# Kernel tuning notes

Hardware: AMD Instinct MI355X
Metric: run time of the kernel (lower is better)

## Reference

```python
import jax, jax.numpy as jnp
import numpy as np

N, NODE_IN, EDGE_IN, H, ROUNDS = 768, 64, 32, 128, 2


def setup_inputs() -> dict:
    key = jax.random.key(0)
    ks = jax.random.split(key, 12)
    node_feats = jax.random.normal(ks[0], (N, NODE_IN), dtype=jnp.float32)
    edge_feats = jax.random.normal(ks[1], (N, N, EDGE_IN), dtype=jnp.float32)
    adj_mask = jax.random.randint(ks[2], (N, N), 0, 2).astype(jnp.float32)
    def lin(k, fan_in, fan_out):
        w = jax.random.normal(k, (fan_in, fan_out), dtype=jnp.float32) / jnp.sqrt(fan_in)
        return w
    return {
        "node_feats": node_feats,
        "edge_feats": edge_feats,
        "adj_mask": adj_mask,
        "Wn": lin(ks[3], NODE_IN, H), "bn": jnp.zeros((H,), jnp.float32),
        "We": lin(ks[4], EDGE_IN, H), "be": jnp.zeros((H,), jnp.float32),
        "Wa": lin(ks[5], 2 * H, H), "ba": jnp.zeros((H,), jnp.float32),
        "Wu": lin(ks[6], 2 * H, H), "bu": jnp.zeros((H,), jnp.float32),
    }


def reference(node_feats, edge_feats, adj_mask, Wn, bn, We, be, Wa, ba, Wu, bu):
    relu = jax.nn.relu
    h = relu(node_feats @ Wn + bn)                      # (N, H)
    e = relu(jnp.einsum('ijf,fk->ijk', edge_feats, We) + be)  # (N, N, H)
    deg = jnp.clip(adj_mask.sum(axis=0), 1.0)[:, None]  # (N, 1) receiver degree
    # Precompute edge contribution to agg_lin once (constant across rounds):
    # concat([sender, e]) @ Wa == sender @ Wa[:H] + e @ Wa[H:]
    e_proj = jnp.einsum('ijh,hk->ijk', e, Wa[H:])       # (N, N, H)
    for _ in range(ROUNDS):
        s_proj = h @ Wa[:H]                              # (N, H) sender part
        msgs = relu(s_proj[:, None, :] + e_proj + ba)    # (N, N, H)
        agg = jnp.einsum('ijk,ij->jk', msgs, adj_mask) / deg  # masked sum over senders i
        h = relu(jnp.concatenate([h, agg], axis=-1) @ Wu + bu)
    graph_emb = h.mean(axis=0)
    return (h, graph_emb)
```

## Files before the change

### kernel.cpp

```cpp
#include <hip/hip_runtime.h>
#include <hip/hip_bf16.h>


typedef __bf16 bf16x8 __attribute__((ext_vector_type(8)));
typedef float f32x4 __attribute__((ext_vector_type(4)));

#define NN 768

static __device__ __forceinline__ unsigned short to_bf16u(float x) {
    return __builtin_bit_cast(unsigned short, (__bf16)x);
}

__global__ __launch_bounds__(256) void k_prep(
                       const float* __restrict__ adj, float* __restrict__ adjT,
                       const float* __restrict__ We, const float* __restrict__ Wa,
                       unsigned short* __restrict__ WeT, unsigned short* __restrict__ Wa2T,
                       const float* __restrict__ nf, const float* __restrict__ Wn,
                       const float* __restrict__ bn, const float* __restrict__ ba,
                       float* __restrict__ h, float* __restrict__ sp) {
    const int b = blockIdx.x, tid = threadIdx.x;
    if (b < 576) {
        __shared__ float tile[32][33];
        int bx = b % 24, by = b / 24;
        int tx = tid & 31, ty = tid >> 5;
#pragma unroll
        for (int yy = 0; yy < 32; yy += 8)
            tile[ty + yy][tx] = adj[(size_t)(by * 32 + ty + yy) * NN + bx * 32 + tx];
        __syncthreads();
#pragma unroll
        for (int yy = 0; yy < 32; yy += 8)
            adjT[(size_t)(bx * 32 + ty + yy) * NN + by * 32 + tx] = tile[tx][ty + yy];
    } else if (b < 656) {
        int g = (b - 576) * 256 + tid;
        if (g < 128 * 32) {
            int c = g >> 5, f = g & 31;
            WeT[g] = to_bf16u(We[f * 128 + c]);
        } else {
            int g2 = g - 128 * 32;
            int c = g2 >> 7, k = g2 & 127;
            Wa2T[g2] = to_bf16u(Wa[(128 + k) * 128 + c]);
        }
    } else if (b < 1040) {
        __shared__ float nf_l[2][64];
        __shared__ float h_l[2][128];
        int row = tid >> 7, t = tid & 127;
        int i = (b - 656) * 2 + row;
        if (t < 64) nf_l[row][t] = nf[i * 64 + t];
        __syncthreads();
        float acc = bn[t];
#pragma unroll 8
        for (int f = 0; f < 64; ++f) acc += nf_l[row][f] * Wn[f * 128 + t];
        acc = fmaxf(acc, 0.f);
        h[i * 128 + t] = acc;
        h_l[row][t] = acc;
        __syncthreads();
        float spv = ba[t];
#pragma unroll 8
        for (int f = 0; f < 128; ++f) spv += h_l[row][f] * Wa[f * 128 + t];
        sp[i * 128 + t] = spv;
    } else {
        if (tid < 128) sp[(size_t)NN * 128 + tid] = -1e30f;
    }
}

__global__ __launch_bounds__(256) void k_big(
    const float* __restrict__ ef, const float* __restrict__ adjT,
    const float* __restrict__ sp, const unsigned short* __restrict__ WeT,
    const unsigned short* __restrict__ Wa2T, const float* __restrict__ be,
    float* __restrict__ agg) {
    __shared__ unsigned short wa2_lds[128 * 128];
    __shared__ __align__(16) unsigned short e_lds[4][16 * 128];
    __shared__ unsigned short idx_lds[NN];
    __shared__ float be_lds[128];
    __shared__ int s_cnt;
    __shared__ float s_invdeg;

    const int tid  = threadIdx.x;
    const int j    = blockIdx.x;
    const int lane = tid & 63;
    const int wv   = tid >> 6;
    const int lg   = lane >> 4;
    const int lr   = lane & 15;

    {
        const int col = tid >> 1;
        const int kb  = (tid & 1) * 64;
#pragma unroll
        for (int m = 0; m < 8; ++m) {
            bf16x8 v = *reinterpret_cast<const bf16x8*>(Wa2T + col * 128 + kb + 8 * m);
            int idx = (col * 128 + kb + 8 * m) ^ ((col & 7) << 3);
            *reinterpret_cast<bf16x8*>(&wa2_lds[idx]) = v;
        }
    }
    if (tid < 128) be_lds[tid] = be[tid];
    bf16x8 bwe[8];
#pragma unroll
    for (int t = 0; t < 8; ++t) {
        int col = 16 * t + lr;
        bwe[t] = *reinterpret_cast<const bf16x8*>(WeT + col * 32 + 8 * lg);
    }
    if (wv == 0) {
        int cnt = 0;
#pragma unroll
        for (int b = 0; b < 12; ++b) {
            float v = adjT[(size_t)j * NN + b * 64 + lane];
            unsigned long long m = __ballot(v != 0.0f);
            if (v != 0.0f) {
                int pos = cnt + __popcll(m & ((1ULL << lane) - 1ULL));
                idx_lds[pos] = (unsigned short)(b * 64 + lane);
            }
            cnt += (int)__popcll(m);
        }
        if (lane == 0) {
            s_cnt = cnt;
            s_invdeg = 1.0f / fmaxf((float)cnt, 1.0f);
        }
    }
    __syncthreads();

    const int cnt = s_cnt;
    const int K = (cnt + 63) >> 6;

    float aggp[8] = {0.f, 0.f, 0.f, 0.f, 0.f, 0.f, 0.f, 0.f};

    float4 a0, a1;
    if (K > 0) {
        int s0 = 16 * wv + lr;
        int r0 = (s0 < cnt) ? (int)idx_lds[s0] : 0;
        const float* p = ef + ((size_t)r0 * NN + j) * 32 + 8 * lg;
        a0 = *reinterpret_cast<const float4*>(p);
        a1 = *reinterpret_cast<const float4*>(p + 4);
    }

    for (int n = 0; n < K; ++n) {
        const int sb = 64 * n + 16 * wv;

        bf16x8 a;
        a[0] = (__bf16)a0.x; a[1] = (__bf16)a0.y; a[2] = (__bf16)a0.z; a[3] = (__bf16)a0.w;
        a[4] = (__bf16)a1.x; a[5] = (__bf16)a1.y; a[6] = (__bf16)a1.z; a[7] = (__bf16)a1.w;

        float4 nx0, nx1;
        if (n + 1 < K) {
            int sn = sb + 64 + lr;
            int rn = (sn < cnt) ? (int)idx_lds[sn] : 0;
            const float* p = ef + ((size_t)rn * NN + j) * 32 + 8 * lg;
            nx0 = *reinterpret_cast<const float4*>(p);
            nx1 = *reinterpret_cast<const float4*>(p + 4);
        }

#pragma unroll
        for (int t = 0; t < 8; ++t) {
            float bb = be_lds[16 * t + lr];
            f32x4 c;
            c[0] = bb; c[1] = bb; c[2] = bb; c[3] = bb;
            f32x4 C1 = __builtin_amdgcn_mfma_f32_16x16x32_bf16(a, bwe[t], c, 0, 0, 0);
#pragma unroll
            for (int r = 0; r < 4; ++r) {
                int row = 4 * lg + r, col = 16 * t + lr;
                int idx = (row * 128 + col) ^ ((row & 7) << 3);
                e_lds[wv][idx] = to_bf16u(fmaxf(C1[r], 0.f));
            }
        }
        bf16x8 ae[4];
#pragma unroll
        for (int s = 0; s < 4; ++s) {
            int idx = (lr * 128 + 32 * s + 8 * lg) ^ ((lr & 7) << 3);
            ae[s] = *reinterpret_cast<const bf16x8*>(&e_lds[wv][idx]);
        }
        int srow[4];
#pragma unroll
        for (int r = 0; r < 4; ++r) {
            int s = sb + 4 * lg + r;
            srow[r] = (s < cnt) ? (int)idx_lds[s] : NN;
        }
#pragma unroll
        for (int t = 0; t < 8; ++t) {
            const int col = 16 * t + lr;
            f32x4 acc;
#pragma unroll
            for (int r = 0; r < 4; ++r)
                acc[r] = sp[(size_t)srow[r] * 128 + col];
#pragma unroll
            for (int s = 0; s < 4; ++s) {
                int widx = (col * 128 + 32 * s + 8 * lg) ^ ((col & 7) << 3);
                bf16x8 bw = *reinterpret_cast<const bf16x8*>(&wa2_lds[widx]);
                acc = __builtin_amdgcn_mfma_f32_16x16x32_bf16(ae[s], bw, acc, 0, 0, 0);
            }
#pragma unroll
            for (int r = 0; r < 4; ++r)
                aggp[t] += fmaxf(acc[r], 0.f);
        }

        if (n + 1 < K) { a0 = nx0; a1 = nx1; }
    }

    float* redw = reinterpret_cast<float*>(&e_lds[wv][0]);
    __syncthreads();
#pragma unroll
    for (int t = 0; t < 8; ++t) {
        float v = aggp[t];
        v += __shfl_xor(v, 16);
        v += __shfl_xor(v, 32);
        if (lane < 16) redw[16 * t + lane] = v;
    }
    __syncthreads();
    if (tid < 128) {
        const float* r0 = reinterpret_cast<const float*>(&e_lds[0][0]);
        const float* r1 = reinterpret_cast<const float*>(&e_lds[1][0]);
        const float* r2 = reinterpret_cast<const float*>(&e_lds[2][0]);
        const float* r3 = reinterpret_cast<const float*>(&e_lds[3][0]);
        agg[(size_t)j * 128 + tid] = (r0[tid] + r1[tid] + r2[tid] + r3[tid]) * s_invdeg;
    }
}

template <int LAST>
__global__ __launch_bounds__(256) void k_upd(
                      const float* __restrict__ h_in, const float* __restrict__ agg,
                      const float* __restrict__ Wu, const float* __restrict__ bu,
                      const float* __restrict__ Wa, const float* __restrict__ ba,
                      float* __restrict__ h_out, float* __restrict__ sp,
                      float* __restrict__ out) {
    __shared__ float buf[2][256];
    __shared__ float hn[2][128];
    const int tid = threadIdx.x;
    const int row = tid >> 7, t = tid & 127;
    const int i = blockIdx.x * 2 + row;
    buf[row][t] = h_in[i * 128 + t];
    buf[row][128 + t] = agg[i * 128 + t];
    __syncthreads();
    float acc = bu[t];
#pragma unroll 8
    for (int f = 0; f < 256; ++f) acc += buf[row][f] * Wu[f * 128 + t];
    acc = fmaxf(acc, 0.f);
    if (LAST) {
        out[i * 128 + t] = acc;
    } else {
        h_out[i * 128 + t] = acc;
        hn[row][t] = acc;
        __syncthreads();
        float spv = ba[t];
#pragma unroll 8
        for (int f = 0; f < 128; ++f) spv += hn[row][f] * Wa[f * 128 + t];
        sp[i * 128 + t] = spv;
    }
}

__global__ __launch_bounds__(64) void k_gemb(const float* __restrict__ out_h, float* __restrict__ out) {
    int c = blockIdx.x, l = threadIdx.x;
    float acc = 0.f;
    for (int i = l; i < NN; i += 64) acc += out_h[(size_t)i * 128 + c];
#pragma unroll
    for (int off = 32; off; off >>= 1) acc += __shfl_down(acc, off);
    if (l == 0) out[NN * 128 + c] = acc * (1.0f / 768.0f);
}

extern "C" void kernel_launch(void* const* d_in, const int* in_sizes, int n_in,
                              void* d_out, int out_size, void* d_ws, size_t ws_size,
                              hipStream_t stream) {
    const float* nf  = (const float*)d_in[0];
    const float* ef  = (const float*)d_in[1];
    const float* adj = (const float*)d_in[2];
    const float* Wn  = (const float*)d_in[3];
    const float* bn  = (const float*)d_in[4];
    const float* We  = (const float*)d_in[5];
    const float* be  = (const float*)d_in[6];
    const float* Wa  = (const float*)d_in[7];
    const float* ba  = (const float*)d_in[8];
    const float* Wu  = (const float*)d_in[9];
    const float* bu  = (const float*)d_in[10];
    float* out = (float*)d_out;

    float* h_buf = (float*)d_ws;
    float* agg   = h_buf + NN * 128;
    float* sp    = agg + NN * 128;
    float* adjT  = sp + (NN + 1) * 128;
    unsigned short* WeT  = (unsigned short*)(adjT + NN * NN);
    unsigned short* Wa2T = WeT + 128 * 32;

    k_prep<<<1041, 256, 0, stream>>>(adj, adjT, We, Wa, WeT, Wa2T, nf, Wn, bn, ba, h_buf, sp);

    k_big<<<NN, 256, 0, stream>>>(ef, adjT, sp, WeT, Wa2T, be, agg);
    k_upd<0><<<NN / 2, 256, 0, stream>>>(h_buf, agg, Wu, bu, Wa, ba, h_buf, sp, out);
    k_big<<<NN, 256, 0, stream>>>(ef, adjT, sp, WeT, Wa2T, be, agg);
    k_upd<1><<<NN / 2, 256, 0, stream>>>(h_buf, agg, Wu, bu, Wa, ba, h_buf, sp, out);

    k_gemb<<<128, 64, 0, stream>>>(out, out);
}
```

Baseline: 143.6 us.

## Split waves into 2x2 row/column grid with register-resident Wa2 and double-buffered edges

Reorganises k_big so the four waves form a 2x2 grid: two sender-row groups times two 64-column halves. Each wave now keeps its slice of Wa[H:] (bwa) in registers, which removes the 32KB LDS copy of Wa2 and the per-iteration LDS reads of weights. The relu(edge @ We) tile is shared between the two column waves through a double-buffered LDS tile. The first GEMM for the next chunk is computed ahead of the second GEMM, synchronised with a per-iteration __syncthreads. The costs are more VGPRs for the 16 weight fragments, a block barrier every iteration, and half as many senders processed per wave-iteration.

```diff
diff --git a/kernel.cpp b/kernel.cpp
--- a/kernel.cpp
+++ b/kernel.cpp
@@ -68,8 +68,7 @@
     const float* __restrict__ sp, const unsigned short* __restrict__ WeT,
     const unsigned short* __restrict__ Wa2T, const float* __restrict__ be,
     float* __restrict__ agg) {
-    __shared__ unsigned short wa2_lds[128 * 128];
-    __shared__ __align__(16) unsigned short e_lds[4][16 * 128];
+    __shared__ __align__(16) unsigned short e_lds[2][2][16 * 128];
     __shared__ unsigned short idx_lds[NN];
     __shared__ float be_lds[128];
     __shared__ int s_cnt;
@@ -79,26 +78,24 @@
     const int j    = blockIdx.x;
     const int lane = tid & 63;
     const int wv   = tid >> 6;
+    const int wr   = wv >> 1;
+    const int wc   = wv & 1;
     const int lg   = lane >> 4;
     const int lr   = lane & 15;
 
-    {
-        const int col = tid >> 1;
-        const int kb  = (tid & 1) * 64;
-#pragma unroll
-        for (int m = 0; m < 8; ++m) {
-            bf16x8 v = *reinterpret_cast<const bf16x8*>(Wa2T + col * 128 + kb + 8 * m);
-            int idx = (col * 128 + kb + 8 * m) ^ ((col & 7) << 3);
-            *reinterpret_cast<bf16x8*>(&wa2_lds[idx]) = v;
-        }
-    }
     if (tid < 128) be_lds[tid] = be[tid];
-    bf16x8 bwe[8];
-#pragma unroll
-    for (int t = 0; t < 8; ++t) {
-        int col = 16 * t + lr;
+
+    bf16x8 bwe[4];
+    bf16x8 bwa[4][4];
+#pragma unroll
+    for (int t = 0; t < 4; ++t) {
+        const int col = 64 * wc + 16 * t + lr;
         bwe[t] = *reinterpret_cast<const bf16x8*>(WeT + col * 32 + 8 * lg);
-    }
+#pragma unroll
+        for (int s = 0; s < 4; ++s)
+            bwa[t][s] = *reinterpret_cast<const bf16x8*>(Wa2T + col * 128 + 32 * s + 8 * lg);
+    }
+
     if (wv == 0) {
         int cnt = 0;
 #pragma unroll
@@ -119,97 +116,94 @@
     __syncthreads();
 
     const int cnt = s_cnt;
-    const int K = (cnt + 63) >> 6;
-
-    float aggp[8] = {0.f, 0.f, 0.f, 0.f, 0.f, 0.f, 0.f, 0.f};
-
-    float4 a0, a1;
-    if (K > 0) {
-        int s0 = 16 * wv + lr;
-        int r0 = (s0 < cnt) ? (int)idx_lds[s0] : 0;
-        const float* p = ef + ((size_t)r0 * NN + j) * 32 + 8 * lg;
-        a0 = *reinterpret_cast<const float4*>(p);
-        a1 = *reinterpret_cast<const float4*>(p + 4);
-    }
-
-    for (int n = 0; n < K; ++n) {
-        const int sb = 64 * n + 16 * wv;
-
+    const int Kc = (cnt + 31) >> 5;
+
+    float aggp[4] = {0.f, 0.f, 0.f, 0.f};
+
+    auto load_ef = [&](int m, float4& x0, float4& x1) {
+        int s = 32 * m + 16 * wr + lr;
+        int r = (s < cnt) ? (int)idx_lds[s] : 0;
+        const float* p = ef + ((size_t)r * NN + j) * 32 + 8 * lg;
+        x0 = *reinterpret_cast<const float4*>(p);
+        x1 = *reinterpret_cast<const float4*>(p + 4);
+    };
+    auto gemm1 = [&](const float4& x0, const float4& x1, int buf) {
         bf16x8 a;
-        a[0] = (__bf16)a0.x; a[1] = (__bf16)a0.y; a[2] = (__bf16)a0.z; a[3] = (__bf16)a0.w;
-        a[4] = (__bf16)a1.x; a[5] = (__bf16)a1.y; a[6] = (__bf16)a1.z; a[7] = (__bf16)a1.w;
-
-        float4 nx0, nx1;
-        if (n + 1 < K) {
-            int sn = sb + 64 + lr;
-            int rn = (sn < cnt) ? (int)idx_lds[sn] : 0;
-            const float* p = ef + ((size_t)rn * NN + j) * 32 + 8 * lg;
-            nx0 = *reinterpret_cast<const float4*>(p);
-            nx1 = *reinterpret_cast<const float4*>(p + 4);
-        }
-
-#pragma unroll
-        for (int t = 0; t < 8; ++t) {
-            float bb = be_lds[16 * t + lr];
+        a[0] = (__bf16)x0.x; a[1] = (__bf16)x0.y; a[2] = (__bf16)x0.z; a[3] = (__bf16)x0.w;
+        a[4] = (__bf16)x1.x; a[5] = (__bf16)x1.y; a[6] = (__bf16)x1.z; a[7] = (__bf16)x1.w;
+#pragma unroll
+        for (int t = 0; t < 4; ++t) {
+            const int col = 64 * wc + 16 * t + lr;
+            float bb = be_lds[col];
             f32x4 c;
             c[0] = bb; c[1] = bb; c[2] = bb; c[3] = bb;
             f32x4 C1 = __builtin_amdgcn_mfma_f32_16x16x32_bf16(a, bwe[t], c, 0, 0, 0);
 #pragma unroll
             for (int r = 0; r < 4; ++r) {
-                int row = 4 * lg + r, col = 16 * t + lr;
+                int row = 4 * lg + r;
                 int idx = (row * 128 + col) ^ ((row & 7) << 3);
-                e_lds[wv][idx] = to_bf16u(fmaxf(C1[r], 0.f));
+                e_lds[buf][wr][idx] = to_bf16u(fmaxf(C1[r], 0.f));
             }
         }
+    };
+
+    float4 c0, c1;
+    if (Kc > 0) {
+        load_ef(0, c0, c1);
+        gemm1(c0, c1, 0);
+        if (Kc > 1) load_ef(1, c0, c1);
+    }
+    __syncthreads();
+
+    for (int n = 0; n < Kc; ++n) {
+        const int b = n & 1;
+        float4 p0, p1;
+        if (n + 2 < Kc) load_ef(n + 2, p0, p1);
+        if (n + 1 < Kc) gemm1(c0, c1, b ^ 1);
+
         bf16x8 ae[4];
 #pragma unroll
         for (int s = 0; s < 4; ++s) {
             int idx = (lr * 128 + 32 * s + 8 * lg) ^ ((lr & 7) << 3);
-            ae[s] = *reinterpret_cast<const bf16x8*>(&e_lds[wv][idx]);
+            ae[s] = *reinterpret_cast<const bf16x8*>(&e_lds[b][wr][idx]);
         }
         int srow[4];
 #pragma unroll
         for (int r = 0; r < 4; ++r) {
-            int s = sb + 4 * lg + r;
+            int s = 32 * n + 16 * wr + 4 * lg + r;
             srow[r] = (s < cnt) ? (int)idx_lds[s] : NN;
         }
 #pragma unroll
-        for (int t = 0; t < 8; ++t) {
-            const int col = 16 * t + lr;
+        for (int t = 0; t < 4; ++t) {
+            const int col = 64 * wc + 16 * t + lr;
             f32x4 acc;
 #pragma unroll
             for (int r = 0; r < 4; ++r)
                 acc[r] = sp[(size_t)srow[r] * 128 + col];
 #pragma unroll
-            for (int s = 0; s < 4; ++s) {
-                int widx = (col * 128 + 32 * s + 8 * lg) ^ ((col & 7) << 3);
-                bf16x8 bw = *reinterpret_cast<const bf16x8*>(&wa2_lds[widx]);
-                acc = __builtin_amdgcn_mfma_f32_16x16x32_bf16(ae[s], bw, acc, 0, 0, 0);
-            }
+            for (int s = 0; s < 4; ++s)
+                acc = __builtin_amdgcn_mfma_f32_16x16x32_bf16(ae[s], bwa[t][s], acc, 0, 0, 0);
 #pragma unroll
             for (int r = 0; r < 4; ++r)
                 aggp[t] += fmaxf(acc[r], 0.f);
         }
 
-        if (n + 1 < K) { a0 = nx0; a1 = nx1; }
-    }
-
-    float* redw = reinterpret_cast<float*>(&e_lds[wv][0]);
-    __syncthreads();
-#pragma unroll
-    for (int t = 0; t < 8; ++t) {
+        if (n + 2 < Kc) { c0 = p0; c1 = p1; }
+        __syncthreads();
+    }
+
+    float* red = reinterpret_cast<float*>(&e_lds[0][0][0]);
+#pragma unroll
+    for (int t = 0; t < 4; ++t) {
         float v = aggp[t];
         v += __shfl_xor(v, 16);
         v += __shfl_xor(v, 32);
-        if (lane < 16) redw[16 * t + lane] = v;
+        if (lane < 16) red[wv * 64 + 16 * t + lane] = v;
     }
     __syncthreads();
     if (tid < 128) {
-        const float* r0 = reinterpret_cast<const float*>(&e_lds[0][0]);
-        const float* r1 = reinterpret_cast<const float*>(&e_lds[1][0]);
-        const float* r2 = reinterpret_cast<const float*>(&e_lds[2][0]);
-        const float* r3 = reinterpret_cast<const float*>(&e_lds[3][0]);
-        agg[(size_t)j * 128 + tid] = (r0[tid] + r1[tid] + r2[tid] + r3[tid]) * s_invdeg;
+        int wcol = tid >> 6, c = tid & 63;
+        agg[(size_t)j * 128 + tid] = (red[wcol * 64 + c] + red[(2 + wcol) * 64 + c]) * s_invdeg;
     }
 }
 
```

Result: no change. 144.1 us (+0.4%).
